# Performance work log

Measured on AMD Instinct MI355X. Metric: run time of the kernel, lower is better.

## Reference

```python
import jax, jax.numpy as jnp
import numpy as np
from jax import lax

B, L = 32, 4096
CFG = [(20, 256, 5, 5), (256, 512, 5, 5), (512, 256, 5, 5), (256, 128, 3, 3), (128, 128, 3, 3)]
H = 16  # GRU hidden
EPS = 1e-5


def setup_inputs() -> dict:
    key = jax.random.key(0)
    ks = iter(jax.random.split(key, 64))
    inp = {"x": jax.random.normal(next(ks), (B, 20, L), jnp.float32)}
    for i, (din, dout, c, _) in enumerate(CFG, 1):
        s = 1.0 / np.sqrt(din * c)
        inp[f"w{i}"] = jax.random.normal(next(ks), (dout, din * c), jnp.float32) * s
        inp[f"b{i}"] = jax.random.normal(next(ks), (dout,), jnp.float32) * 0.01
        inp[f"g{i}"] = jax.random.uniform(next(ks), (dout,), jnp.float32, 0.5, 1.5)
        inp[f"bb{i}"] = jax.random.normal(next(ks), (dout,), jnp.float32) * 0.1
        inp[f"m{i}"] = jax.random.normal(next(ks), (dout,), jnp.float32) * 0.1
        inp[f"v{i}"] = jax.random.uniform(next(ks), (dout,), jnp.float32, 0.5, 1.5)
    for l, din in enumerate([128, H]):
        s = 1.0 / np.sqrt(H)
        inp[f"wih{l}"] = jax.random.normal(next(ks), (3 * H, din), jnp.float32) * s
        inp[f"whh{l}"] = jax.random.normal(next(ks), (3 * H, H), jnp.float32) * s
        inp[f"bih{l}"] = jax.random.normal(next(ks), (3 * H,), jnp.float32) * 0.01
        inp[f"bhh{l}"] = jax.random.normal(next(ks), (3 * H,), jnp.float32) * 0.01
    return inp


def _tdnn(x, w, b, g, bb, m, v, c, d):
    # x: (B, L, Din). Dilated unfold -> (B, Lout, c*Din), then linear+relu+BN(eval).
    Lo = x.shape[1] - (c - 1) * d
    f = jnp.concatenate([lax.dynamic_slice_in_dim(x, i * d, Lo, axis=1) for i in range(c)], axis=-1)
    y = jnp.maximum(jnp.einsum('blk,ok->blo', f, w) + b, 0.0)
    return (y - m) * (g * lax.rsqrt(v + EPS)) + bb


def _gru_layer(x, wih, whh, bih, bhh):
    # PyTorch GRU cell; gate order (r, z, n). x: (B, T, Din) -> (B, T, H)
    b = x.shape[0]
    gi = jnp.einsum('btd,gd->btg', x, wih) + bih  # precompute input projections

    def step(h, gi_t):
        gh = h @ whh.T + bhh
        ir, iz, inn = jnp.split(gi_t, 3, axis=-1)
        hr, hz, hn = jnp.split(gh, 3, axis=-1)
        r = jax.nn.sigmoid(ir + hr)
        z = jax.nn.sigmoid(iz + hz)
        n = jnp.tanh(inn + r * hn)
        h = (1.0 - z) * n + z * h
        return h, h

    h0 = jnp.zeros((b, whh.shape[1]), x.dtype)
    _, ys = lax.scan(step, h0, jnp.swapaxes(gi, 0, 1))
    return jnp.swapaxes(ys, 0, 1)


def reference(x,
              w1, b1, g1, bb1, m1, v1,
              w2, b2, g2, bb2, m2, v2,
              w3, b3, g3, bb3, m3, v3,
              w4, b4, g4, bb4, m4, v4,
              w5, b5, g5, bb5, m5, v5,
              wih0, whh0, bih0, bhh0,
              wih1, whh1, bih1, bhh1):
    h = jnp.swapaxes(x, 1, 2)  # (B, L, 20)
    tp = [(w1, b1, g1, bb1, m1, v1), (w2, b2, g2, bb2, m2, v2), (w3, b3, g3, bb3, m3, v3),
          (w4, b4, g4, bb4, m4, v4), (w5, b5, g5, bb5, m5, v5)]
    for (w, b, g, bb, m, v), (_, _, c, d) in zip(tp, CFG):
        h = _tdnn(h, w, b, g, bb, m, v, c, d)
    h = h.reshape(h.shape[0], -1, 128)
    h = _gru_layer(h, wih0, whh0, bih0, bhh0)
    h = _gru_layer(h, wih1, whh1, bih1, bhh1)
    return h.reshape(h.shape[0], -1)
```

## Files before the change

kernel.cpp:

```cpp
#include <hip/hip_runtime.h>

typedef __bf16 bf16_t;
typedef __bf16 bf16x8 __attribute__((ext_vector_type(8)));
typedef float f32x4 __attribute__((ext_vector_type(4)));
typedef __fp16 f16_t;
typedef __fp16 f16x2 __attribute__((ext_vector_type(2)));
typedef __fp16 f16x8 __attribute__((ext_vector_type(8)));
typedef int i32x4 __attribute__((ext_vector_type(4)));

#define EPSBN 1e-5f
#define LOG2E 1.4426950408889634f

__device__ __forceinline__ void gload16(const void* g, void* l) {
  __builtin_amdgcn_global_load_lds(
      (const __attribute__((address_space(1))) void*)g,
      (__attribute__((address_space(3))) void*)l, 16, 0, 0);
}

__device__ __forceinline__ int h2i(f16x2 x) { union { int i; f16x2 h; } u; u.h = x; return u.i; }

__device__ __forceinline__ float exp2x(float x) {
#if __has_builtin(__builtin_amdgcn_exp2f)
  return __builtin_amdgcn_exp2f(x);
#else
  return exp2f(x);
#endif
}
__device__ __forceinline__ float rcpx(float x) {
#if __has_builtin(__builtin_amdgcn_rcpf)
  return __builtin_amdgcn_rcpf(x);
#else
  return 1.0f / x;
#endif
}

__global__ __launch_bounds__(256) void pack_w_kernel(
    const float* __restrict__ w1, const float* __restrict__ w2,
    const float* __restrict__ w3, const float* __restrict__ w4,
    const float* __restrict__ w5,
    bf16_t* __restrict__ p1, bf16_t* __restrict__ p2, bf16_t* __restrict__ p3,
    bf16_t* __restrict__ p4, bf16_t* __restrict__ p5)
{
  const int idx = blockIdx.x * 256 + threadIdx.x;
  switch (blockIdx.y) {
    case 0:
      if (idx < 256 * 160) {
        int o = idx / 160, k = idx % 160, tap = k / 32, ch = k % 32;
        p1[idx] = (bf16_t)((ch < 20) ? w1[o * 100 + tap * 20 + ch] : 0.0f);
      }
      break;
    case 1: if (idx < 512 * 1280) p2[idx] = (bf16_t)w2[idx]; break;
    case 2: if (idx < 256 * 2560) p3[idx] = (bf16_t)w3[idx]; break;
    case 3: if (idx < 128 * 768)  p4[idx] = (bf16_t)w4[idx]; break;
    default: if (idx < 128 * 384) p5[idx] = (bf16_t)w5[idx]; break;
  }
}

__global__ __launch_bounds__(256) void pack_x_kernel(
    const float* __restrict__ x, bf16_t* __restrict__ xp)
{
  __shared__ __align__(16) bf16_t Ls[256 * 32];
  const int tid = threadIdx.x;
  const int b = blockIdx.y;
  const int l0 = blockIdx.x * 256;
  bf16x8 z = {};
  #pragma unroll
  for (int i = 0; i < 4; ++i) ((bf16x8*)Ls)[tid + i * 256] = z;
  __syncthreads();
  #pragma unroll
  for (int ch = 0; ch < 20; ++ch) {
    float v = x[((size_t)b * 20 + ch) * 4096 + l0 + tid];
    Ls[tid * 32 + ch] = (bf16_t)v;
  }
  __syncthreads();
  bf16x8* dst = (bf16x8*)(xp + ((size_t)b * 4096 + l0) * 32);
  #pragma unroll
  for (int i = 0; i < 4; ++i) dst[tid + i * 256] = ((bf16x8*)Ls)[tid + i * 256];
}

template <int DIN, int C, int DIL, bool OUTF32>
__global__ __launch_bounds__(256, 2) void tdnn_gemm(
    const bf16_t* __restrict__ X, const bf16_t* __restrict__ W,
    const float* __restrict__ bias, const float* __restrict__ gg,
    const float* __restrict__ bb, const float* __restrict__ mm,
    const float* __restrict__ vv,
    bf16_t* __restrict__ Yb, float* __restrict__ Yf,
    const int Lin, const int Lo, const int N)
{
  __shared__ __align__(16) bf16_t As[128 * 32];
  __shared__ __align__(16) bf16_t Bs[128 * 32];
  const int tid = threadIdx.x;
  const int wave = tid >> 6;
  const int lane = tid & 63;
  const int l0 = blockIdx.x * 128;
  const int n0 = blockIdx.y * 128;
  const int b = blockIdx.z;
  const int lm = lane & 15;
  const int quad = lane >> 4;
  const int wm = (wave >> 1) * 64;
  const int wn = (wave & 1) * 64;
  constexpr int Ktot = C * DIN;

  const int srow = wave * 32 + (lane >> 2);
  const int scol = (lane & 3) * 8;

  const int rA0 = min(l0 + srow, Lo - 1);
  const int rA1 = min(l0 + srow + 16, Lo - 1);

  const bf16_t* Xb = X + (size_t)b * Lin * DIN;
  const bf16_t* xg0 = Xb + (size_t)rA0 * DIN + scol;
  const bf16_t* xg1 = Xb + (size_t)rA1 * DIN + scol;
  const bf16_t* wg0 = W + (size_t)(n0 + srow) * Ktot + scol;
  const bf16_t* wg1 = W + (size_t)(n0 + srow + 16) * Ktot + scol;

  bf16_t* AsW = &As[(wave * 32) * 32];
  bf16_t* BsW = &Bs[(wave * 32) * 32];

  f32x4 acc[4][4];
  f32x4 zz = {};
  #pragma unroll
  for (int i = 0; i < 4; ++i)
    #pragma unroll
    for (int j = 0; j < 4; ++j) acc[i][j] = zz;

  for (int tap = 0; tap < C; ++tap) {
    const bf16_t* xa0 = xg0 + (size_t)tap * DIL * DIN;
    const bf16_t* xa1 = xg1 + (size_t)tap * DIL * DIN;
    const bf16_t* wa0 = wg0 + tap * DIN;
    const bf16_t* wa1 = wg1 + tap * DIN;
    for (int kc = 0; kc < DIN / 32; ++kc) {
      gload16(xa0 + kc * 32, AsW);
      gload16(xa1 + kc * 32, AsW + 16 * 32);
      gload16(wa0 + kc * 32, BsW);
      gload16(wa1 + kc * 32, BsW + 16 * 32);
      __syncthreads();
      bf16x8 av[4], bv[4];
      #pragma unroll
      for (int mt = 0; mt < 4; ++mt)
        av[mt] = *(const bf16x8*)&As[(wm + mt * 16 + lm) * 32 + quad * 8];
      #pragma unroll
      for (int nt = 0; nt < 4; ++nt)
        bv[nt] = *(const bf16x8*)&Bs[(wn + nt * 16 + lm) * 32 + quad * 8];
      #pragma unroll
      for (int mt = 0; mt < 4; ++mt)
        #pragma unroll
        for (int nt = 0; nt < 4; ++nt)
          acc[mt][nt] = __builtin_amdgcn_mfma_f32_16x16x32_bf16(av[mt], bv[nt], acc[mt][nt], 0, 0, 0);
      __syncthreads();
    }
  }

  #pragma unroll
  for (int nt = 0; nt < 4; ++nt) {
    const int col = n0 + wn + nt * 16 + lm;
    const float sc = gg[col] * rsqrtf(vv[col] + EPSBN);
    const float sh = bb[col] - mm[col] * sc;
    const float bi = bias[col];
    #pragma unroll
    for (int mt = 0; mt < 4; ++mt) {
      const int rbase = l0 + wm + mt * 16 + quad * 4;
      #pragma unroll
      for (int r = 0; r < 4; ++r) {
        const int row = rbase + r;
        if (row < Lo) {
          float val = fmaxf(acc[mt][nt][r] + bi, 0.0f) * sc + sh;
          const size_t oi = ((size_t)b * Lo + row) * N + col;
          if constexpr (OUTF32) Yf[oi] = val;
          else                  Yb[oi] = (bf16_t)val;
        }
      }
    }
  }
}

template <int DIN, int C, int DIL, bool OUTF32>
__global__ __launch_bounds__(256, 2) void tdnn_gemm64(
    const bf16_t* __restrict__ X, const bf16_t* __restrict__ W,
    const float* __restrict__ bias, const float* __restrict__ gg,
    const float* __restrict__ bb, const float* __restrict__ mm,
    const float* __restrict__ vv,
    bf16_t* __restrict__ Yb, float* __restrict__ Yf,
    const int Lin, const int Lo, const int N)
{
  __shared__ __align__(16) bf16_t As[128 * 64];
  __shared__ __align__(16) bf16_t Bs[128 * 64];
  const int tid = threadIdx.x;
  const int wave = tid >> 6;
  const int lane = tid & 63;
  const int l0 = blockIdx.x * 128;
  const int n0 = blockIdx.y * 128;
  const int b = blockIdx.z;
  const int lm = lane & 15;
  const int quad = lane >> 4;
  const int wm = (wave >> 1) * 64;
  const int wn = (wave & 1) * 64;
  constexpr int Ktot = C * DIN;

  const int srow8 = lane >> 3;
  const int sc = ((lane & 7) ^ srow8) * 8;

  const bf16_t* Xb = X + (size_t)b * Lin * DIN;
  const bf16_t* xsrc[4];
  const bf16_t* wsrc[4];
  #pragma unroll
  for (int it = 0; it < 4; ++it) {
    const int r = wave * 32 + 8 * it + srow8;
    const int ra = min(l0 + r, Lo - 1);
    xsrc[it] = Xb + (size_t)ra * DIN + sc;
    wsrc[it] = W + (size_t)(n0 + r) * Ktot + sc;
  }
  bf16_t* AsW = &As[wave * 32 * 64];
  bf16_t* BsW = &Bs[wave * 32 * 64];

  f32x4 acc[4][4];
  f32x4 zz = {};
  #pragma unroll
  for (int i = 0; i < 4; ++i)
    #pragma unroll
    for (int j = 0; j < 4; ++j) acc[i][j] = zz;

  for (int tap = 0; tap < C; ++tap) {
    const size_t xoff = (size_t)tap * DIL * DIN;
    const int woff = tap * DIN;
    for (int kc = 0; kc < DIN / 64; ++kc) {
      #pragma unroll
      for (int it = 0; it < 4; ++it) {
        gload16(xsrc[it] + xoff + kc * 64, AsW + it * 512);
        gload16(wsrc[it] + woff + kc * 64, BsW + it * 512);
      }
      __syncthreads();
      #pragma unroll
      for (int ks = 0; ks < 2; ++ks) {
        bf16x8 av[4], bv[4];
        #pragma unroll
        for (int mt = 0; mt < 4; ++mt) {
          const int row = wm + mt * 16 + lm;
          av[mt] = *(const bf16x8*)&As[row * 64 + (((ks * 4 + quad) ^ (row & 7)) * 8)];
        }
        #pragma unroll
        for (int nt = 0; nt < 4; ++nt) {
          const int row = wn + nt * 16 + lm;
          bv[nt] = *(const bf16x8*)&Bs[row * 64 + (((ks * 4 + quad) ^ (row & 7)) * 8)];
        }
        #pragma unroll
        for (int mt = 0; mt < 4; ++mt)
          #pragma unroll
          for (int nt = 0; nt < 4; ++nt)
            acc[mt][nt] = __builtin_amdgcn_mfma_f32_16x16x32_bf16(av[mt], bv[nt], acc[mt][nt], 0, 0, 0);
      }
      __syncthreads();
    }
  }

  #pragma unroll
  for (int nt = 0; nt < 4; ++nt) {
    const int col = n0 + wn + nt * 16 + lm;
    const float sc2 = gg[col] * rsqrtf(vv[col] + EPSBN);
    const float sh = bb[col] - mm[col] * sc2;
    const float bi = bias[col];
    #pragma unroll
    for (int mt = 0; mt < 4; ++mt) {
      const int rbase = l0 + wm + mt * 16 + quad * 4;
      #pragma unroll
      for (int r = 0; r < 4; ++r) {
        const int row = rbase + r;
        if (row < Lo) {
          float val = fmaxf(acc[mt][nt][r] + bi, 0.0f) * sc2 + sh;
          const size_t oi = ((size_t)b * Lo + row) * N + col;
          if constexpr (OUTF32) Yf[oi] = val;
          else                  Yb[oi] = (bf16_t)val;
        }
      }
    }
  }
}

__global__ __launch_bounds__(256, 2) void gi0_kernel(
    const float* __restrict__ A5, const float* __restrict__ wih,
    const float* __restrict__ bih, float* __restrict__ GI, const int T)
{
  __shared__ __align__(16) float Xs[64 * 132];
  __shared__ __align__(16) float Ws[48 * 132];
  const int tid = threadIdx.x;
  const int b = blockIdx.y, t0 = blockIdx.x * 64;
  for (int c = tid; c < 48 * 32; c += 256) {
    int j = c >> 5, k4 = c & 31;
    *(float4*)&Ws[j * 132 + k4 * 4] = *(const float4*)&wih[j * 128 + k4 * 4];
  }
  for (int c = tid; c < 64 * 32; c += 256) {
    int r = c >> 5, k4 = c & 31;
    int tt = min(t0 + r, T - 1);
    *(float4*)&Xs[r * 132 + k4 * 4] = *(const float4*)&A5[((size_t)b * T + tt) * 128 + k4 * 4];
  }
  __syncthreads();
  const int tl = tid >> 2, jg = tid & 3;
  float acc[12];
  #pragma unroll
  for (int i = 0; i < 12; ++i) acc[i] = 0.0f;
  for (int k = 0; k < 128; k += 4) {
    float4 xv = *(const float4*)&Xs[tl * 132 + k];
    #pragma unroll
    for (int jj = 0; jj < 12; ++jj) {
      float4 wv = *(const float4*)&Ws[(jg * 12 + jj) * 132 + k];
      acc[jj] += xv.x * wv.x + xv.y * wv.y + xv.z * wv.z + xv.w * wv.w;
    }
  }
  const int t = t0 + tl;
  if (t < T) {
    float* dst = &GI[((size_t)b * T + t) * 64];
    #pragma unroll
    for (int jj = 0; jj < 12; ++jj) {
      const int row = jg * 12 + jj;
      const float s = (row >= 32) ? (2.0f * LOG2E) : (-LOG2E);
      dst[(row & 15) * 4 + (row >> 4)] = (acc[jj] + bih[row]) * s;
    }
  }
}

__global__ __launch_bounds__(64, 1) void gru_kernel(
    const float* __restrict__ GI,
    const float* __restrict__ whh0, const float* __restrict__ bhh0,
    const float* __restrict__ wih1, const float* __restrict__ bih1,
    const float* __restrict__ whh1, const float* __restrict__ bhh1,
    float* __restrict__ out, const int T)
{
  const int b = blockIdx.x;
  const int lane = threadIdx.x;
  const int u = lane & 15;
  const bool L1 = ((lane >> 4) & 1) != 0;
  const bool STORE1 = (lane >= 16 && lane < 32);

  const int ks = (lane >> 4) * 8;
  constexpr float SL = -LOG2E;
  constexpr float SN = 2.0f * LOG2E;

  f16x8 B1, B2, B3, B4, B5, B6, B7;
  #pragma unroll
  for (int j = 0; j < 8; ++j) {
    const int k = ks + j;
    const bool lo = (k < 16);
    const int kk = lo ? k : (k - 16);
    B1[j] = (f16_t)(lo ? SL * whh0[(0  + u) * 16 + kk] : 0.0f);
    B2[j] = (f16_t)(lo ? SL * whh0[(16 + u) * 16 + kk] : 0.0f);
    B3[j] = (f16_t)(lo ? SN * whh0[(32 + u) * 16 + kk] : 0.0f);
    B4[j] = (f16_t)(SL * (lo ? wih1[(0  + u) * 16 + kk] : whh1[(0  + u) * 16 + kk]));
    B5[j] = (f16_t)(SL * (lo ? wih1[(16 + u) * 16 + kk] : whh1[(16 + u) * 16 + kk]));
    B6[j] = (f16_t)(lo ? SN * wih1[(32 + u) * 16 + kk] : 0.0f);
    B7[j] = (f16_t)(lo ? 0.0f : SN * whh1[(32 + u) * 16 + kk]);
  }
  const float c1 = SL * bhh0[u], c2 = SL * bhh0[16 + u], c3 = SN * bhh0[32 + u];
  const float c4b = SL * (bih1[u] + bhh1[u]), c5b = SL * (bih1[16 + u] + bhh1[16 + u]);
  const float c6 = SN * bih1[32 + u], c7 = SN * bhh1[32 + u];
  const f32x4 C1 = {c1, c1, c1, c1}, C2 = {c2, c2, c2, c2}, C3 = {c3, c3, c3, c3};
  const f32x4 C4 = {c4b, c4b, c4b, c4b}, C5 = {c5b, c5b, c5b, c5b};
  const f32x4 C6 = {c6, c6, c6, c6}, C7 = {c7, c7, c7, c7};

  const int ab = (lane >> 4) * 32;
  const int ad0 = ab, ad1 = ab + 8, ad2 = ab + 16, ad3 = ab + 24;

  const float* gib = GI + (size_t)b * T * 64 + u * 4;
  float4 g[8];
  #pragma unroll
  for (int p = 0; p < 8; ++p)
    g[p] = *(const float4*)(gib + (size_t)p * 64);

  float hreg = 0.f;
  i32x4 aw = {0, 0, 0, 0};
  float* outp = out + (size_t)b * T * 16 + u;

  const int nb = (T + 8) / 8;
  for (int body = 0; body < nb; ++body) {
    const int base = body * 8;
    #pragma unroll
    for (int p = 0; p < 8; ++p) {
      const int i = base + p;
      const float4 gv = g[p];
      g[p] = *(const float4*)(gib + (size_t)(i + 8) * 64);

      const f16x8 A = __builtin_bit_cast(f16x8, aw);
      const f32x4 D1 = __builtin_amdgcn_mfma_f32_16x16x32_f16(A, B1, C1, 0, 0, 0);
      const f32x4 D2 = __builtin_amdgcn_mfma_f32_16x16x32_f16(A, B2, C2, 0, 0, 0);
      const f32x4 D3 = __builtin_amdgcn_mfma_f32_16x16x32_f16(A, B3, C3, 0, 0, 0);
      const f32x4 D4 = __builtin_amdgcn_mfma_f32_16x16x32_f16(A, B4, C4, 0, 0, 0);
      const f32x4 D5 = __builtin_amdgcn_mfma_f32_16x16x32_f16(A, B5, C5, 0, 0, 0);
      const f32x4 D6 = __builtin_amdgcn_mfma_f32_16x16x32_f16(A, B6, C6, 0, 0, 0);
      const f32x4 D7 = __builtin_amdgcn_mfma_f32_16x16x32_f16(A, B7, C7, 0, 0, 0);

      const float pre_r = L1 ? D4[0] : (gv.x + D1[0]);
      const float pre_z = L1 ? D5[0] : (gv.y + D2[0]);
      const float aIn   = L1 ? D6[0] : gv.z;
      const float aRn   = L1 ? D7[0] : D3[0];

      const float r = rcpx(1.0f + exp2x(pre_r));
      const float z = rcpx(1.0f + exp2x(pre_z));
      const float e = exp2x(fmaf(r, aRn, aIn));
      const float n = fmaf(-2.0f, rcpx(e + 1.0f), 1.0f);
      float hnew = fmaf(z, hreg - n, n);

      if (i == 0 && L1) hnew = 0.f;
      hreg = hnew;

      const int hi = __float_as_int(hreg);
#if __has_builtin(__builtin_amdgcn_mov_dpp)
      const float hp = __int_as_float(__builtin_amdgcn_mov_dpp(hi, 0xB1, 0xF, 0xF, true));
#else
      const float hp = __shfl_xor(hreg, 1);
#endif
      const int pki = h2i(__builtin_amdgcn_cvt_pkrtz(hreg, hp));
      aw[0] = __builtin_amdgcn_ds_bpermute(ad0, pki);
      aw[1] = __builtin_amdgcn_ds_bpermute(ad1, pki);
      aw[2] = __builtin_amdgcn_ds_bpermute(ad2, pki);
      aw[3] = __builtin_amdgcn_ds_bpermute(ad3, pki);

      if (STORE1 && i > 0 && i <= T)
        outp[(size_t)(i - 1) * 16] = hnew;
    }
  }
}

extern "C" void kernel_launch(void* const* d_in, const int* in_sizes, int n_in,
                              void* d_out, int out_size, void* d_ws, size_t ws_size,
                              hipStream_t stream) {
  (void)in_sizes; (void)n_in; (void)out_size; (void)ws_size;
  const float* x = (const float*)d_in[0];
  const float* w1 = (const float*)d_in[1];  const float* b1 = (const float*)d_in[2];
  const float* g1 = (const float*)d_in[3];  const float* bb1 = (const float*)d_in[4];
  const float* m1 = (const float*)d_in[5];  const float* v1 = (const float*)d_in[6];
  const float* w2 = (const float*)d_in[7];  const float* b2 = (const float*)d_in[8];
  const float* g2 = (const float*)d_in[9];  const float* bb2 = (const float*)d_in[10];
  const float* m2 = (const float*)d_in[11]; const float* v2 = (const float*)d_in[12];
  const float* w3 = (const float*)d_in[13]; const float* b3 = (const float*)d_in[14];
  const float* g3 = (const float*)d_in[15]; const float* bb3 = (const float*)d_in[16];
  const float* m3 = (const float*)d_in[17]; const float* v3 = (const float*)d_in[18];
  const float* w4 = (const float*)d_in[19]; const float* b4 = (const float*)d_in[20];
  const float* g4 = (const float*)d_in[21]; const float* bb4 = (const float*)d_in[22];
  const float* m4 = (const float*)d_in[23]; const float* v4 = (const float*)d_in[24];
  const float* w5 = (const float*)d_in[25]; const float* b5 = (const float*)d_in[26];
  const float* g5 = (const float*)d_in[27]; const float* bb5 = (const float*)d_in[28];
  const float* m5 = (const float*)d_in[29]; const float* v5 = (const float*)d_in[30];
  const float* wih0 = (const float*)d_in[31];
  const float* whh0 = (const float*)d_in[32];
  const float* bih0 = (const float*)d_in[33];
  const float* bhh0 = (const float*)d_in[34];
  const float* wih1 = (const float*)d_in[35];
  const float* whh1 = (const float*)d_in[36];
  const float* bih1 = (const float*)d_in[37];
  const float* bhh1 = (const float*)d_in[38];

  char* ws = (char*)d_ws;
  size_t off = 0;
  auto alloc = [&](size_t bytes) {
    size_t r = off;
    off = (off + bytes + 255) & ~(size_t)255;
    return r;
  };
  bf16_t* p1 = (bf16_t*)(ws + alloc((size_t)256 * 160 * 2));
  bf16_t* p2 = (bf16_t*)(ws + alloc((size_t)512 * 1280 * 2));
  bf16_t* p3 = (bf16_t*)(ws + alloc((size_t)256 * 2560 * 2));
  bf16_t* p4 = (bf16_t*)(ws + alloc((size_t)128 * 768 * 2));
  bf16_t* p5 = (bf16_t*)(ws + alloc((size_t)128 * 384 * 2));
  bf16_t* xp = (bf16_t*)(ws + alloc((size_t)32 * 4096 * 32 * 2));
  char* bufA = ws + alloc((size_t)32 * 4076 * 256 * 2);
  char* bufB = ws + alloc((size_t)32 * 4056 * 512 * 2);

  bf16_t* a1 = (bf16_t*)bufA;
  bf16_t* a2 = (bf16_t*)bufB;
  bf16_t* a3 = (bf16_t*)bufA;
  bf16_t* a4 = (bf16_t*)bufB;
  float*  a5 = (float*)bufA;
  float*  gi = (float*)bufB;

  hipLaunchKernelGGL(pack_w_kernel, dim3(2560, 5), dim3(256), 0, stream,
                     w1, w2, w3, w4, w5, p1, p2, p3, p4, p5);
  hipLaunchKernelGGL(pack_x_kernel, dim3(16, 32), dim3(256), 0, stream, x, xp);

  hipLaunchKernelGGL((tdnn_gemm<32, 5, 5, false>), dim3(32, 2, 32), dim3(256), 0, stream,
                     xp, p1, b1, g1, bb1, m1, v1, a1, (float*)nullptr, 4096, 4076, 256);
  hipLaunchKernelGGL((tdnn_gemm64<256, 5, 5, false>), dim3(32, 4, 32), dim3(256), 0, stream,
                     a1, p2, b2, g2, bb2, m2, v2, a2, (float*)nullptr, 4076, 4056, 512);
  hipLaunchKernelGGL((tdnn_gemm64<512, 5, 5, false>), dim3(32, 2, 32), dim3(256), 0, stream,
                     a2, p3, b3, g3, bb3, m3, v3, a3, (float*)nullptr, 4056, 4036, 256);
  hipLaunchKernelGGL((tdnn_gemm64<256, 3, 3, false>), dim3(32, 1, 32), dim3(256), 0, stream,
                     a3, p4, b4, g4, bb4, m4, v4, a4, (float*)nullptr, 4036, 4030, 128);
  hipLaunchKernelGGL((tdnn_gemm64<128, 3, 3, true>), dim3(32, 1, 32), dim3(256), 0, stream,
                     a4, p5, b5, g5, bb5, m5, v5, (bf16_t*)nullptr, a5, 4030, 4024, 128);

  hipLaunchKernelGGL(gi0_kernel, dim3(63, 32), dim3(256), 0, stream, a5, wih0, bih0, gi, 4024);
  hipLaunchKernelGGL(gru_kernel, dim3(32), dim3(64), 0, stream,
                     gi, whh0, bhh0, wih1, bih1, whh1, bhh1, (float*)d_out, 4024);
}
```

Baseline: 1.499 ms.

## Double-buffer LDS tiles in TDNN GEMM to overlap loads with MFMA

The TDNN GEMM kernel now uses two LDS buffers for the A and B tiles and flattens the tap and k-chunk loops into a single pipelined loop. The next tile's global-to-LDS loads are issued before the current tile's MFMA work, and the barriers drop from two per iteration to one. The aim is to hide global load latency behind matrix compute. The cost is twice the shared memory per block, which may limit occupancy, and correctness relies on the async LDS loads completing before the barrier.

After: 1.574 ms. 5.0% more time.

```diff
diff --git a/kernel.cpp b/kernel.cpp
--- a/kernel.cpp
+++ b/kernel.cpp
@@ -182,8 +182,10 @@
     bf16_t* __restrict__ Yb, float* __restrict__ Yf,
     const int Lin, const int Lo, const int N)
 {
-  __shared__ __align__(16) bf16_t As[128 * 64];
-  __shared__ __align__(16) bf16_t Bs[128 * 64];
+  constexpr int KC = DIN / 64;
+  constexpr int NT = C * KC;
+  __shared__ __align__(16) bf16_t As[2][128 * 64];
+  __shared__ __align__(16) bf16_t Bs[2][128 * 64];
   const int tid = threadIdx.x;
   const int wave = tid >> 6;
   const int lane = tid & 63;
@@ -209,8 +211,6 @@
     xsrc[it] = Xb + (size_t)ra * DIN + sc;
     wsrc[it] = W + (size_t)(n0 + r) * Ktot + sc;
   }
-  bf16_t* AsW = &As[wave * 32 * 64];
-  bf16_t* BsW = &Bs[wave * 32 * 64];
 
   f32x4 acc[4][4];
   f32x4 zz = {};
@@ -219,37 +219,45 @@
     #pragma unroll
     for (int j = 0; j < 4; ++j) acc[i][j] = zz;
 
-  for (int tap = 0; tap < C; ++tap) {
-    const size_t xoff = (size_t)tap * DIL * DIN;
-    const int woff = tap * DIN;
-    for (int kc = 0; kc < DIN / 64; ++kc) {
-      #pragma unroll
-      for (int it = 0; it < 4; ++it) {
-        gload16(xsrc[it] + xoff + kc * 64, AsW + it * 512);
-        gload16(wsrc[it] + woff + kc * 64, BsW + it * 512);
+  auto stage = [&](int t, int buf) {
+    const int tap = t / KC, kc = t - tap * KC;
+    const size_t xo = (size_t)tap * DIL * DIN + kc * 64;
+    const int    wo = tap * DIN + kc * 64;
+    bf16_t* AsW = &As[buf][wave * 32 * 64];
+    bf16_t* BsW = &Bs[buf][wave * 32 * 64];
+    #pragma unroll
+    for (int it = 0; it < 4; ++it) {
+      gload16(xsrc[it] + xo, AsW + it * 512);
+      gload16(wsrc[it] + wo, BsW + it * 512);
+    }
+  };
+
+  stage(0, 0);
+  __syncthreads();
+
+  for (int t = 0; t < NT; ++t) {
+    const int cur = t & 1;
+    if (t + 1 < NT) stage(t + 1, cur ^ 1);
+    #pragma unroll
+    for (int ks = 0; ks < 2; ++ks) {
+      bf16x8 av[4], bv[4];
+      #pragma unroll
+      for (int mt = 0; mt < 4; ++mt) {
+        const int row = wm + mt * 16 + lm;
+        av[mt] = *(const bf16x8*)&As[cur][row * 64 + (((ks * 4 + quad) ^ (row & 7)) * 8)];
       }
-      __syncthreads();
-      #pragma unroll
-      for (int ks = 0; ks < 2; ++ks) {
-        bf16x8 av[4], bv[4];
+      #pragma unroll
+      for (int nt = 0; nt < 4; ++nt) {
+        const int row = wn + nt * 16 + lm;
+        bv[nt] = *(const bf16x8*)&Bs[cur][row * 64 + (((ks * 4 + quad) ^ (row & 7)) * 8)];
+      }
+      #pragma unroll
+      for (int mt = 0; mt < 4; ++mt)
         #pragma unroll
-        for (int mt = 0; mt < 4; ++mt) {
-          const int row = wm + mt * 16 + lm;
-          av[mt] = *(const bf16x8*)&As[row * 64 + (((ks * 4 + quad) ^ (row & 7)) * 8)];
-        }
-        #pragma unroll
-        for (int nt = 0; nt < 4; ++nt) {
-          const int row = wn + nt * 16 + lm;
-          bv[nt] = *(const bf16x8*)&Bs[row * 64 + (((ks * 4 + quad) ^ (row & 7)) * 8)];
-        }
-        #pragma unroll
-        for (int mt = 0; mt < 4; ++mt)
-          #pragma unroll
-          for (int nt = 0; nt < 4; ++nt)
-            acc[mt][nt] = __builtin_amdgcn_mfma_f32_16x16x32_bf16(av[mt], bv[nt], acc[mt][nt], 0, 0, 0);
-      }
-      __syncthreads();
-    }
+        for (int nt = 0; nt < 4; ++nt)
+          acc[mt][nt] = __builtin_amdgcn_mfma_f32_16x16x32_bf16(av[mt], bv[nt], acc[mt][nt], 0, 0, 0);
+    }
+    __syncthreads();
   }
 
   #pragma unroll
```
